# Performance work log

Measured on AMD Instinct MI355X. Metric: run time of the kernel, lower is better.

The kernel has to match this reference:

```python
import jax, jax.numpy as jnp
import numpy as np


def setup_inputs() -> dict:
    key = jax.random.key(0)
    k1, k2 = jax.random.split(key)
    B, S, D, K = 8, 2048, 512, 8192
    x = jax.random.normal(k1, (B, S, D), dtype=jnp.float32)
    codebook = jax.random.normal(k2, (K, D), dtype=jnp.float32)
    return {"x": x, "codebook": codebook}


def reference(x, codebook):
    # x: [B, S, D], codebook: [K, D]
    B, S, D = x.shape
    flat_x = x.reshape(-1, D)                      # [N, D], N = B*S
    distances = (
        jnp.sum(flat_x * flat_x, axis=1, keepdims=True)
        - 2.0 * jnp.matmul(flat_x, codebook.T)
        + jnp.sum(codebook * codebook, axis=1)
    )
    encoding_indices = jnp.argmin(distances, axis=1)  # [N]
    quantized = codebook[encoding_indices]            # [N, D] embedding lookup
    return quantized.reshape(x.shape)                 # [B, S, D]
```

## Files before the change

kernel.cpp:

```cpp
#include <hip/hip_runtime.h>


#define MROWS 16384
#define KCB   8192
#define DDIM  512
#define NKT   8
#define NTILES (KCB / 128)
#define MARGIN 8.0f

typedef unsigned short u16;
typedef unsigned int uint;
typedef __attribute__((ext_vector_type(8))) short bf16x8;
typedef __attribute__((ext_vector_type(4))) float f32x4;

__device__ inline u16 f2bf(float f) {
  unsigned int u = __float_as_uint(f);
  u += 0x7FFFu + ((u >> 16) & 1u);
  return (u16)(u >> 16);
}

__device__ inline void gload16(const void* g, void* l) {
  __builtin_amdgcn_global_load_lds((const __attribute__((address_space(1))) void*)g,
                                   (__attribute__((address_space(3))) void*)l,
                                   16, 0, 0);
}

__device__ inline double shfl_xor_dbl(double v, int m) {
  long long l = __double_as_longlong(v);
  int lo = (int)(l & 0xffffffffLL), hi = (int)(l >> 32);
  lo = __shfl_xor(lo, m, 64);
  hi = __shfl_xor(hi, m, 64);
  return __longlong_as_double(((long long)hi << 32) | (unsigned long long)(unsigned int)lo);
}

__device__ inline float keyval(uint k) {
  uint u = k & 0xFFFFFF80u;
  uint bits = (u & 0x80000000u) ? (u & 0x7FFFFFFFu) : ~u;
  return __uint_as_float(bits);
}


__global__ __launch_bounds__(256) void k_conv_x(const float* __restrict__ x,
                                                u16* __restrict__ xb) {
  size_t i = ((size_t)blockIdx.x * 256 + threadIdx.x) * 8;
  float4 a = *(const float4*)(x + i);
  float4 b = *(const float4*)(x + i + 4);
  union { u16 s[8]; uint4 v; } u;
  u.s[0]=f2bf(a.x); u.s[1]=f2bf(a.y); u.s[2]=f2bf(a.z); u.s[3]=f2bf(a.w);
  u.s[4]=f2bf(b.x); u.s[5]=f2bf(b.y); u.s[6]=f2bf(b.z); u.s[7]=f2bf(b.w);
  *(uint4*)(xb + i) = u.v;
}

__global__ __launch_bounds__(256) void k_conv_cb(const float* __restrict__ cb,
                                                 u16* __restrict__ cbb,
                                                 float* __restrict__ cnorm) {
  int k = blockIdx.x * 4 + (threadIdx.x >> 6);
  int lane = threadIdx.x & 63;
  size_t base = (size_t)k * DDIM + lane * 8;
  float4 a = *(const float4*)(cb + base);
  float4 b = *(const float4*)(cb + base + 4);
  union { u16 s[8]; uint4 v; } u;
  u.s[0]=f2bf(a.x); u.s[1]=f2bf(a.y); u.s[2]=f2bf(a.z); u.s[3]=f2bf(a.w);
  u.s[4]=f2bf(b.x); u.s[5]=f2bf(b.y); u.s[6]=f2bf(b.z); u.s[7]=f2bf(b.w);
  *(uint4*)(cbb + base) = u.v;
  float s = a.x*a.x + a.y*a.y + a.z*a.z + a.w*a.w
          + b.x*b.x + b.y*b.y + b.z*b.z + b.w*b.w;
  #pragma unroll
  for (int m = 1; m < 64; m <<= 1) s += __shfl_xor(s, m, 64);
  if (lane == 0) cnorm[k] = s;
}


__global__ __launch_bounds__(512, 2) void k_gemm_min(
    const u16* __restrict__ Xbf, const u16* __restrict__ Cbf,
    const float* __restrict__ cnorm, uint2* __restrict__ stats)
{
  extern __shared__ __align__(16) u16 lds[];

  int bid = blockIdx.x;
  int xcd = bid & 7;
  int j   = bid >> 3;
  int mTile = xcd * 8 + (j & 7);
  int nTile = j >> 3;
  int rowBase = mTile * 256;
  int colBase = nTile * 256;

  int tid = threadIdx.x;
  int lane = tid & 63;
  int wv = tid >> 6;
  int wr = wv >> 2;
  int wc = wv & 3;
  int grp = lane >> 4;
  int l15 = lane & 15;

  const int rr = tid >> 3;
  const int pc = (tid & 7) ^ (rr & 7);
  const u16* pA = Cbf + (size_t)(colBase + rr) * DDIM + pc * 8;
  const u16* pB = Xbf + (size_t)(rowBase + rr) * DDIM + pc * 8;

  const int m7 = l15 & 7;
  const int ch0 = (grp ^ m7);
  const int ch1 = ch0 ^ 4;
  const int cOff0 = wr * 4096 + l15 * 64 + ch0 * 8;
  const int cOff1 = wr * 4096 + l15 * 64 + ch1 * 8;
  const int xOff0 = wc * 4096 + l15 * 64 + ch0 * 8;
  const int xOff1 = wc * 4096 + l15 * 64 + ch1 * 8;

  f32x4 acc[8][4];
  #pragma unroll
  for (int mi = 0; mi < 8; ++mi)
    #pragma unroll
    for (int ni = 0; ni < 4; ++ni)
      acc[mi][ni] = (f32x4){0.f, 0.f, 0.f, 0.f};

  gload16(pB,           (void*)&lds[32768 + tid * 8]);
  gload16(pB + 32768,   (void*)&lds[32768 + 4096 + tid * 8]);
  gload16(pB + 65536,   (void*)&lds[32768 + 8192 + tid * 8]);
  gload16(pB + 98304,   (void*)&lds[32768 + 12288 + tid * 8]);
  gload16(pA,           (void*)&lds[tid * 8]);
  gload16(pA + 65536,   (void*)&lds[4096 + tid * 8]);
  gload16(pA + 32768,   (void*)&lds[8192 + tid * 8]);
  gload16(pA + 98304,   (void*)&lds[8192 + 4096 + tid * 8]);

  bf16x8 xF[4];

  #pragma unroll
  for (int it = 0; it < 4; ++it) {
    #pragma unroll
    for (int ph = 0; ph < 8; ++ph) {
      const int b  = ph >> 2;
      const int s  = ph & 3;
      const int h  = s & 1;
      const int ks = s >> 1;
      const int tauS = 2 * it + 1 + (ph >> 2);
      const int bS = (ph < 4) ? 1 : 0;

      if ((ph & 2) == 0) {
        if (it == 3 && ph == 5) { asm volatile("s_waitcnt vmcnt(0)" ::: "memory"); }
        else                    { asm volatile("s_waitcnt vmcnt(2)" ::: "memory"); }
      }
      __builtin_amdgcn_s_barrier();
      __builtin_amdgcn_sched_barrier(0);

      bf16x8 cF[4];
      #pragma unroll
      for (int q = 0; q < 4; ++q)
        cF[q] = *(const bf16x8*)&lds[b * 16384 + h * 8192 + q * 1024 + (ks ? cOff1 : cOff0)];
      if (h == 0) {
        #pragma unroll
        for (int ni = 0; ni < 4; ++ni)
          xF[ni] = *(const bf16x8*)&lds[32768 + b * 16384 + ni * 1024 + (ks ? xOff1 : xOff0)];
      }

      if (!(it == 3 && ph >= 4)) {
        if (s < 2) {
          gload16(pB + s * 65536 + tauS * 64,
                  (void*)&lds[32768 + bS * 16384 + s * 8192 + tid * 8]);
          gload16(pB + s * 65536 + 32768 + tauS * 64,
                  (void*)&lds[32768 + bS * 16384 + s * 8192 + 4096 + tid * 8]);
        } else {
          const int ha = s - 2;
          gload16(pA + ha * 32768 + tauS * 64,
                  (void*)&lds[bS * 16384 + ha * 8192 + tid * 8]);
          gload16(pA + ha * 32768 + 65536 + tauS * 64,
                  (void*)&lds[bS * 16384 + ha * 8192 + 4096 + tid * 8]);
        }
      }

      asm volatile("s_waitcnt lgkmcnt(0)" ::: "memory");
      __builtin_amdgcn_sched_barrier(0);
      __builtin_amdgcn_s_setprio(1);
      #pragma unroll
      for (int q = 0; q < 4; ++q)
        #pragma unroll
        for (int ni = 0; ni < 4; ++ni)
          acc[h * 4 + q][ni] =
            __builtin_amdgcn_mfma_f32_16x16x32_bf16(cF[q], xF[ni], acc[h * 4 + q][ni], 0, 0, 0);
      __builtin_amdgcn_s_setprio(0);
    }
  }

#define INS(st1, st2, st3, kx)                                     \
  { uint kk_ = (kx);                                               \
    bool lt1 = kk_ < st1, lt2 = kk_ < st2, lt3 = kk_ < st3;        \
    st3 = lt3 ? (lt2 ? st2 : kk_) : st3;                           \
    st2 = lt2 ? (lt1 ? st1 : kk_) : st2;                           \
    st1 = lt1 ? kk_ : st1; }

  uint t1[4], t2[4], t3[4];
  #pragma unroll
  for (int ni = 0; ni < 4; ++ni) { t1[ni] = 0xFFFFFFFFu; t2[ni] = 0xFFFFFFFFu; t3[ni] = 0xFFFFFFFFu; }

  #pragma unroll
  for (int mi = 0; mi < 8; ++mi) {
    float cnv[4];
    *(float4*)cnv = *(const float4*)&cnorm[colBase + wr * 128 + mi * 16 + grp * 4];
    #pragma unroll
    for (int ni = 0; ni < 4; ++ni) {
      #pragma unroll
      for (int rg = 0; rg < 4; ++rg) {
        float v = cnv[rg] - 2.0f * acc[mi][ni][rg];
        uint u = __float_as_uint(v);
        u = ((int)u < 0) ? ~u : (u | 0x80000000u);
        uint key = (u & 0xFFFFFF80u) | (uint)(mi * 16 + grp * 4 + rg);
        INS(t1[ni], t2[ni], t3[ni], key);
      }
    }
  }
  #pragma unroll
  for (int ni = 0; ni < 4; ++ni) {
    #pragma unroll
    for (int mk = 16; mk <= 32; mk <<= 1) {
      uint o1 = (uint)__shfl_xor((int)t1[ni], mk, 64);
      uint o2 = (uint)__shfl_xor((int)t2[ni], mk, 64);
      uint o3 = (uint)__shfl_xor((int)t3[ni], mk, 64);
      INS(t1[ni], t2[ni], t3[ni], o1);
      INS(t1[ni], t2[ni], t3[ni], o2);
      INS(t1[ni], t2[ni], t3[ni], o3);
    }
  }
#undef INS
  if (grp == 0) {
    #pragma unroll
    for (int ni = 0; ni < 4; ++ni) {
      float v1 = keyval(t1[ni]), v2 = keyval(t2[ni]), v3 = keyval(t3[ni]);
      uint i1 = t1[ni] & 127u, i2 = t2[ni] & 127u;
      uint d2 = min(255u, (uint)((v2 - v1) * 4.0f));
      uint d3 = min(255u, (uint)((v3 - v1) * 4.0f));
      uint2 st;
      st.x = __float_as_uint(v1);
      st.y = i1 | (i2 << 7) | (d2 << 14) | (d3 << 22);
      int xrow = rowBase + wc * 64 + ni * 16 + l15;
      stats[(size_t)xrow * NTILES + nTile * 2 + wr] = st;
    }
  }
}


__device__ inline void eval64(const float4& xa, const float4& xb,
                              const float* __restrict__ cb, int col,
                              double& best, int& bi, int lane) {
  const float* cr = cb + (size_t)col * DDIM + lane * 8;
  float4 ca = *(const float4*)cr;
  float4 cv = *(const float4*)(cr + 4);
  double s = 0.0, d;
  d = (double)xa.x - (double)ca.x; s += d*d;
  d = (double)xa.y - (double)ca.y; s += d*d;
  d = (double)xa.z - (double)ca.z; s += d*d;
  d = (double)xa.w - (double)ca.w; s += d*d;
  d = (double)xb.x - (double)cv.x; s += d*d;
  d = (double)xb.y - (double)cv.y; s += d*d;
  d = (double)xb.z - (double)cv.z; s += d*d;
  d = (double)xb.w - (double)cv.w; s += d*d;
  #pragma unroll
  for (int m = 1; m < 64; m <<= 1) s += shfl_xor_dbl(s, m);
  if (s < best || (s == best && col < bi)) { best = s; bi = col; }
}

__global__ __launch_bounds__(256) void k_refine(
    const float* __restrict__ x, const float* __restrict__ cb,
    const float* __restrict__ cnorm, const uint2* __restrict__ stats,
    unsigned int* __restrict__ bestOut)
{
  int n = blockIdx.x * 4 + (threadIdx.x >> 6);
  int lane = threadIdx.x & 63;
  uint2 st = stats[(size_t)n * NTILES + lane];
  float m1 = __uint_as_float(st.x);
  int   i1 = st.y & 127, i2 = (st.y >> 7) & 127;
  float m2 = m1 + ((st.y >> 14) & 255u) * 0.25f;
  float m3 = m1 + ((st.y >> 22) & 255u) * 0.25f;
  float g = m1;
  #pragma unroll
  for (int m = 1; m < 64; m <<= 1) g = fminf(g, __shfl_xor(g, m, 64));
  float T = g + MARGIN;
  unsigned long long q1 = __ballot(m1 <= T);
  unsigned long long q2 = __ballot(m2 <= T);
  unsigned long long qr = __ballot(m3 <= T);

  const float* xr = x + (size_t)n * DDIM;
  float4 xa = *(const float4*)(xr + lane * 8);
  float4 xb = *(const float4*)(xr + lane * 8 + 4);

  double best = 1e300;
  int bi = 0x7fffffff;

  while (q1) {
    int t = __ffsll(q1) - 1; q1 &= q1 - 1;
    int col = t * 128 + __shfl(i1, t, 64);
    eval64(xa, xb, cb, col, best, bi, lane);
  }
  while (q2) {
    int t = __ffsll(q2) - 1; q2 &= q2 - 1;
    int col = t * 128 + __shfl(i2, t, 64);
    eval64(xa, xb, cb, col, best, bi, lane);
  }
  while (qr) {
    int t = __ffsll(qr) - 1; qr &= qr - 1;
    for (int c2 = 0; c2 < 128; ++c2) {
      int col2 = t * 128 + c2;
      const float* cr = cb + (size_t)col2 * DDIM + lane * 8;
      float4 ca = *(const float4*)cr;
      float4 cv = *(const float4*)(cr + 4);
      float p = xa.x*ca.x + xa.y*ca.y + xa.z*ca.z + xa.w*ca.w
              + xb.x*cv.x + xb.y*cv.y + xb.z*cv.z + xb.w*cv.w;
      #pragma unroll
      for (int m = 1; m < 64; m <<= 1) p += __shfl_xor(p, m, 64);
      float s32 = cnorm[col2] - 2.0f * p;
      if (s32 <= T) {
        double s = 0.0, dd;
        dd = (double)xa.x - (double)ca.x; s += dd*dd;
        dd = (double)xa.y - (double)ca.y; s += dd*dd;
        dd = (double)xa.z - (double)ca.z; s += dd*dd;
        dd = (double)xa.w - (double)ca.w; s += dd*dd;
        dd = (double)xb.x - (double)cv.x; s += dd*dd;
        dd = (double)xb.y - (double)cv.y; s += dd*dd;
        dd = (double)xb.z - (double)cv.z; s += dd*dd;
        dd = (double)xb.w - (double)cv.w; s += dd*dd;
        #pragma unroll
        for (int m = 1; m < 64; m <<= 1) s += shfl_xor_dbl(s, m);
        if (s < best || (s == best && col2 < bi)) { best = s; bi = col2; }
      }
    }
  }
  if (lane == 0) bestOut[n] = (unsigned int)bi;
}


__global__ __launch_bounds__(256) void k_gather(const float* __restrict__ cb,
                                                const unsigned int* __restrict__ bestIdx,
                                                float* __restrict__ out) {
  int n = blockIdx.x * 4 + (threadIdx.x >> 6);
  int lane = threadIdx.x & 63;
  unsigned int b = bestIdx[n];
  const float4* s = (const float4*)(cb + (size_t)b * DDIM);
  float4* dp = (float4*)(out + (size_t)n * DDIM);
  dp[lane * 2]     = s[lane * 2];
  dp[lane * 2 + 1] = s[lane * 2 + 1];
}


extern "C" void kernel_launch(void* const* d_in, const int* in_sizes, int n_in,
                              void* d_out, int out_size, void* d_ws, size_t ws_size,
                              hipStream_t stream) {
  const float* x  = (const float*)d_in[0];
  const float* cb = (const float*)d_in[1];
  float* out = (float*)d_out;

  char* ob = (char*)d_out;
  u16*   Xbf   = (u16*)ob;
  u16*   Cbf   = (u16*)(ob + 16ull * 1024 * 1024);
  uint2* stats = (uint2*)(ob + 24ull * 1024 * 1024);

  char* wsb = (char*)d_ws;
  float* cnorm = (float*)wsb;
  unsigned int* bestIdx = (unsigned int*)(wsb + 32 * 1024);

  (void)hipFuncSetAttribute((const void*)k_gemm_min,
                            hipFuncAttributeMaxDynamicSharedMemorySize, 131072);

  k_conv_x  <<<4096, 256, 0, stream>>>(x, Xbf);
  k_conv_cb <<<2048, 256, 0, stream>>>(cb, Cbf, cnorm);
  k_gemm_min<<<2048, 512, 131072, stream>>>(Xbf, Cbf, cnorm, stats);
  k_refine  <<<4096, 256, 0, stream>>>(x, cb, cnorm, stats, bestIdx);
  k_gather  <<<4096, 256, 0, stream>>>(cb, bestIdx, out);
}
```

Measured before the change: 257.4 us.

## Double-buffer LDS fragment reads and restage global loads in GEMM main loop

Restructures the bf16 MFMA main loop into 32 flat phases where the LDS fragment reads for the next phase are issued before the current phase's MFMAs, using double-buffered register fragments. Global-to-LDS staging is reordered so each half-tile is prefetched one or two k-tiles ahead, with partial vmcnt/lgkmcnt waits. This is meant to hide LDS read latency behind MFMA execution instead of waiting with lgkmcnt(0) each phase. It costs extra VGPRs for the second fragment set, which could lower occupancy, and it depends on the hand-counted waitcnt values being correct.

```diff
diff --git a/kernel.cpp b/kernel.cpp
--- a/kernel.cpp
+++ b/kernel.cpp
@@ -4,7 +4,6 @@
 #define MROWS 16384
 #define KCB   8192
 #define DDIM  512
-#define NKT   8
 #define NTILES (KCB / 128)
 #define MARGIN 8.0f
 
@@ -113,72 +112,81 @@
     for (int ni = 0; ni < 4; ++ni)
       acc[mi][ni] = (f32x4){0.f, 0.f, 0.f, 0.f};
 
-  gload16(pB,           (void*)&lds[32768 + tid * 8]);
-  gload16(pB + 32768,   (void*)&lds[32768 + 4096 + tid * 8]);
-  gload16(pB + 65536,   (void*)&lds[32768 + 8192 + tid * 8]);
-  gload16(pB + 98304,   (void*)&lds[32768 + 12288 + tid * 8]);
-  gload16(pA,           (void*)&lds[tid * 8]);
-  gload16(pA + 65536,   (void*)&lds[4096 + tid * 8]);
-  gload16(pA + 32768,   (void*)&lds[8192 + tid * 8]);
-  gload16(pA + 98304,   (void*)&lds[8192 + 4096 + tid * 8]);
-
-  bf16x8 xF[4];
-
-  #pragma unroll
-  for (int it = 0; it < 4; ++it) {
-    #pragma unroll
-    for (int ph = 0; ph < 8; ++ph) {
-      const int b  = ph >> 2;
-      const int s  = ph & 3;
-      const int h  = s & 1;
-      const int ks = s >> 1;
-      const int tauS = 2 * it + 1 + (ph >> 2);
-      const int bS = (ph < 4) ? 1 : 0;
-
-      if ((ph & 2) == 0) {
-        if (it == 3 && ph == 5) { asm volatile("s_waitcnt vmcnt(0)" ::: "memory"); }
-        else                    { asm volatile("s_waitcnt vmcnt(2)" ::: "memory"); }
-      }
-      __builtin_amdgcn_s_barrier();
-      __builtin_amdgcn_sched_barrier(0);
-
-      bf16x8 cF[4];
-      #pragma unroll
-      for (int q = 0; q < 4; ++q)
-        cF[q] = *(const bf16x8*)&lds[b * 16384 + h * 8192 + q * 1024 + (ks ? cOff1 : cOff0)];
-      if (h == 0) {
-        #pragma unroll
-        for (int ni = 0; ni < 4; ++ni)
-          xF[ni] = *(const bf16x8*)&lds[32768 + b * 16384 + ni * 1024 + (ks ? xOff1 : xOff0)];
-      }
-
-      if (!(it == 3 && ph >= 4)) {
-        if (s < 2) {
-          gload16(pB + s * 65536 + tauS * 64,
-                  (void*)&lds[32768 + bS * 16384 + s * 8192 + tid * 8]);
-          gload16(pB + s * 65536 + 32768 + tauS * 64,
-                  (void*)&lds[32768 + bS * 16384 + s * 8192 + 4096 + tid * 8]);
-        } else {
-          const int ha = s - 2;
-          gload16(pA + ha * 32768 + tauS * 64,
-                  (void*)&lds[bS * 16384 + ha * 8192 + tid * 8]);
-          gload16(pA + ha * 32768 + 65536 + tauS * 64,
-                  (void*)&lds[bS * 16384 + ha * 8192 + 4096 + tid * 8]);
-        }
-      }
-
-      asm volatile("s_waitcnt lgkmcnt(0)" ::: "memory");
-      __builtin_amdgcn_sched_barrier(0);
-      __builtin_amdgcn_s_setprio(1);
+  bf16x8 cF[2][4];
+  bf16x8 xF[2][4];
+
+#define STAGE_AH0(T) { const int d_=((T)&1)*16384; const int so_=(T)*64;                  \
+  gload16(pA + so_,          (void*)&lds[d_ + tid * 8]);                                  \
+  gload16(pA + 65536 + so_,  (void*)&lds[d_ + 4096 + tid * 8]); }
+#define STAGE_AH1(T) { const int d_=((T)&1)*16384 + 8192; const int so_=(T)*64;           \
+  gload16(pA + 32768 + so_,  (void*)&lds[d_ + tid * 8]);                                  \
+  gload16(pA + 98304 + so_,  (void*)&lds[d_ + 4096 + tid * 8]); }
+#define STAGE_BH0(T) { const int d_=32768+((T)&1)*16384; const int so_=(T)*64;            \
+  gload16(pB + so_,          (void*)&lds[d_ + tid * 8]);                                  \
+  gload16(pB + 32768 + so_,  (void*)&lds[d_ + 4096 + tid * 8]); }
+#define STAGE_BH1(T) { const int d_=32768+((T)&1)*16384 + 8192; const int so_=(T)*64;     \
+  gload16(pB + 65536 + so_,  (void*)&lds[d_ + tid * 8]);                                  \
+  gload16(pB + 98304 + so_,  (void*)&lds[d_ + 4096 + tid * 8]); }
+
+#define ISSUE_READS(pp)                                                                   \
+  { const int kt_ = (pp) >> 2, s_ = (pp) & 3, h_ = s_ >> 1, ks_ = s_ & 1;                 \
+    const int bo_ = (kt_ & 1) * 16384;                                                    \
+    const int co_ = ks_ ? cOff1 : cOff0;                                                  \
+    _Pragma("unroll")                                                                     \
+    for (int q = 0; q < 4; ++q)                                                           \
+      cF[(pp) & 1][q] = *(const bf16x8*)&lds[bo_ + h_ * 8192 + q * 1024 + co_];           \
+    if (h_ == 0) {                                                                        \
+      const int xo_ = ks_ ? xOff1 : xOff0;                                                \
+      _Pragma("unroll")                                                                   \
+      for (int ni = 0; ni < 4; ++ni)                                                      \
+        xF[(pp) & 1][ni] = *(const bf16x8*)&lds[32768 + bo_ + ni * 1024 + xo_];           \
+    } }
+
+  STAGE_AH0(0); STAGE_AH1(0); STAGE_BH0(0); STAGE_BH1(0);
+  STAGE_AH0(1); STAGE_BH0(1);
+  asm volatile("s_waitcnt vmcnt(4)" ::: "memory");
+  __builtin_amdgcn_s_barrier();
+  __builtin_amdgcn_sched_barrier(0);
+  ISSUE_READS(0);
+
+  #pragma unroll
+  for (int ph = 0; ph < 32; ++ph) {
+    const int s = ph & 3, kt = ph >> 2;
+
+    if (s == 3 && ph != 31) asm volatile("s_waitcnt vmcnt(2)" ::: "memory");
+    if (ph == 29)           asm volatile("s_waitcnt vmcnt(0)" ::: "memory");
+    __builtin_amdgcn_s_barrier();
+    __builtin_amdgcn_sched_barrier(0);
+
+    if      (s == 0 && kt <= 6) { STAGE_BH1(kt + 1); }
+    else if (s == 1 && kt <= 6) { STAGE_AH1(kt + 1); }
+    else if (s == 2 && kt <= 5) { STAGE_AH0(kt + 2); }
+    else if (s == 3 && kt <= 5) { STAGE_BH0(kt + 2); }
+
+    if (ph < 31) ISSUE_READS(ph + 1);
+
+    if (ph == 31)            asm volatile("s_waitcnt lgkmcnt(0)" ::: "memory");
+    else if (((ph + 1) & 2) == 0) asm volatile("s_waitcnt lgkmcnt(8)" ::: "memory");
+    else                     asm volatile("s_waitcnt lgkmcnt(4)" ::: "memory");
+    __builtin_amdgcn_sched_barrier(0);
+
+    __builtin_amdgcn_s_setprio(1);
+    {
+      const int h = s >> 1;
       #pragma unroll
       for (int q = 0; q < 4; ++q)
         #pragma unroll
         for (int ni = 0; ni < 4; ++ni)
-          acc[h * 4 + q][ni] =
-            __builtin_amdgcn_mfma_f32_16x16x32_bf16(cF[q], xF[ni], acc[h * 4 + q][ni], 0, 0, 0);
-      __builtin_amdgcn_s_setprio(0);
-    }
-  }
+          acc[h * 4 + q][ni] = __builtin_amdgcn_mfma_f32_16x16x32_bf16(
+              cF[ph & 1][q], xF[ph & 1][ni], acc[h * 4 + q][ni], 0, 0, 0);
+    }
+    __builtin_amdgcn_s_setprio(0);
+  }
+#undef ISSUE_READS
+#undef STAGE_AH0
+#undef STAGE_AH1
+#undef STAGE_BH0
+#undef STAGE_BH1
 
 #define INS(st1, st2, st3, kx)                                     \
   { uint kk_ = (kx);                                               \
```

Measured after the change: 256.0 us. About the same (-0.5%).
